# Kernel optimization log

Measured on AMD Instinct MI355X. Metric: run time of the kernel, lower is better.

The kernel has to match this reference:

```python
import jax, jax.numpy as jnp
import numpy as np

N_MODELS = 64
IN_F = 256
OUT_F = 256
BATCH = 8192


def setup_inputs() -> dict:
    key = jax.random.key(0)
    kx, kw, kb, ki = jax.random.split(key, 4)
    x = jax.random.normal(kx, (BATCH, OUT_F), dtype=jnp.float32)
    idxs = jax.random.randint(ki, (BATCH,), 0, N_MODELS, dtype=jnp.int64)
    # learned parameters (torch inits them to zeros; we use random so grads/outputs are nontrivial)
    w = jax.random.normal(kw, (N_MODELS, IN_F, OUT_F), dtype=jnp.float32) * 0.02
    b = jax.random.normal(kb, (N_MODELS, OUT_F), dtype=jnp.float32) * 0.02
    return {"x": x, "idxs": idxs, "w": w, "b": b}


def reference(x, idxs, w, b):
    # torch: baddbmm(b[idxs,:,None], w[idxs], x[:,:,None]).squeeze(-1) -> relu
    # y[n, i] = b[idxs[n], i] + sum_o w[idxs[n], i, o] * x[n, o]
    wg = w[idxs]                      # (B, in, out) gathered per-sample weights
    bg = b[idxs]                      # (B, out)
    y = jnp.einsum('bio,bo->bi', wg, x) + bg
    return jax.nn.relu(y)
```

## Files before the change

kernel.cpp:

```cpp
#include <hip/hip_runtime.h>
#include <stdint.h>


#define N_MODELS 64
#define IN_F     256
#define OUT_F    256
#define BATCH    8192
#define BM       128
#define BN       128
#define PKX      264

typedef __bf16 bf16x8 __attribute__((ext_vector_type(8)));
typedef float  f32x4  __attribute__((ext_vector_type(4)));
typedef __attribute__((address_space(3))) uint32_t lds_u32;
typedef const __attribute__((address_space(1))) uint32_t glb_u32;

__device__ __forceinline__ void dma16(const void* g, void* l) {
  __builtin_amdgcn_global_load_lds((glb_u32*)g, (lds_u32*)l, 16, 0, 0);
}

__device__ __forceinline__ bf16x8 pack8(float4 a, float4 b) {
  bf16x8 o;
  o[0] = (__bf16)a.x; o[1] = (__bf16)a.y; o[2] = (__bf16)a.z; o[3] = (__bf16)a.w;
  o[4] = (__bf16)b.x; o[5] = (__bf16)b.y; o[6] = (__bf16)b.z; o[7] = (__bf16)b.w;
  return o;
}

__global__ __launch_bounds__(1024) void compact_kernel(
    const int* __restrict__ idxs, int* __restrict__ rid_g,
    int* __restrict__ cnt_g) {
  const int model = blockIdx.x;
  const int t     = threadIdx.x;
  const int lane  = t & 63;
  const int wv    = t >> 6;
  __shared__ int wsum[16];

  const int4* ip = (const int4*)idxs + t * 2;
  int4 iv0 = ip[0], iv1 = ip[1];

  int cnt = (iv0.x == model) + (iv0.y == model) + (iv0.z == model) + (iv0.w == model)
          + (iv1.x == model) + (iv1.y == model) + (iv1.z == model) + (iv1.w == model);
  int inc = cnt;
#pragma unroll
  for (int d = 1; d < 64; d <<= 1) {
    int u = __shfl_up(inc, d);
    if (lane >= d) inc += u;
  }
  if (lane == 63) wsum[wv] = inc;
  __syncthreads();
  int wpre = 0, total = 0;
#pragma unroll
  for (int j = 0; j < 16; ++j) {
    int s = wsum[j];
    total += s;
    if (j < wv) wpre += s;
  }
  int off = wpre + inc - cnt;
  int* rg = rid_g + model * 256;
  {
    int n0 = t * 8;
    if (iv0.x == model) { if ((unsigned)off < 256u) rg[off] = n0 + 0; ++off; }
    if (iv0.y == model) { if ((unsigned)off < 256u) rg[off] = n0 + 1; ++off; }
    if (iv0.z == model) { if ((unsigned)off < 256u) rg[off] = n0 + 2; ++off; }
    if (iv0.w == model) { if ((unsigned)off < 256u) rg[off] = n0 + 3; ++off; }
    if (iv1.x == model) { if ((unsigned)off < 256u) rg[off] = n0 + 4; ++off; }
    if (iv1.y == model) { if ((unsigned)off < 256u) rg[off] = n0 + 5; ++off; }
    if (iv1.z == model) { if ((unsigned)off < 256u) rg[off] = n0 + 6; ++off; }
    if (iv1.w == model) { if ((unsigned)off < 256u) rg[off] = n0 + 7; ++off; }
  }
  if (t < 256 && t >= total) rg[t] = -1;
  if (t == 0) cnt_g[model] = total;
}

__global__ __launch_bounds__(1024) void gemm_kernel(
    const float* __restrict__ x, const float* __restrict__ w,
    const float* __restrict__ bias_g, float* __restrict__ out,
    const int* __restrict__ rid_g, const int* __restrict__ cnt_g) {
  const int b     = (blockIdx.x & 7) * 32 + (blockIdx.x >> 3);
  const int model = b >> 2;
  const int s     = (b >> 1) & 1;
  const int i0    = (b & 1) * BN;
  const int t     = threadIdx.x;
  const int lane  = t & 63;
  const int wv    = t >> 6;

  __shared__ float w_lds[2][BM][64];
  __shared__ unsigned short a_lds[BM][PKX];
  __shared__ int rid[BM];

  const int total = cnt_g[model];
  if (s * BM >= total) return;

  if (t < BM) rid[t] = rid_g[model * 256 + s * BM + t];
  const int rwx  = t >> 3;
  const int hx   = t & 7;
  const int srow = rid_g[model * 256 + s * BM + rwx];

  const float* wbase = w + (size_t)model * (IN_F * OUT_F) + (size_t)i0 * IN_F;
  const int l_r = lane >> 4;
  const int l_c = lane & 15;
#define W_DMA(q, buf)                                                        \
  {                                                                          \
    _Pragma("unroll")                                                        \
    for (int j = 0; j < 2; ++j) {                                            \
      const int r0 = wv * 8 + j * 4;                                         \
      const int rr = r0 + l_r;                                               \
      const float* gs = wbase + (size_t)rr * IN_F + (q) * 64                 \
                        + ((l_c ^ (rr & 7)) << 2);                           \
      dma16(gs, &w_lds[buf][r0][0]);                                         \
    }                                                                        \
  }

  W_DMA(0, 0)
  W_DMA(1, 1)

  const float* xrow = x + (size_t)(srow < 0 ? 0 : srow) * IN_F + hx * 32;
  {
    float4 tx[8];
#pragma unroll
    for (int j = 0; j < 8; ++j) tx[j] = *(const float4*)(xrow + j * 4);
#pragma unroll
    for (int j = 0; j < 4; ++j)
      *(bf16x8*)&a_lds[rwx][hx * 32 + j * 8] = pack8(tx[2 * j], tx[2 * j + 1]);
  }

  const int wm   = (wv & 3) * 32;
  const int wn   = (wv >> 2) * 32;
  const int col  = lane & 15;
  const int quad = lane >> 4;
  float bv[2];
  const float* bp = bias_g + model * OUT_F + i0 + wn + col;
#pragma unroll
  for (int nt = 0; nt < 2; ++nt) bv[nt] = bp[nt * 16];

  __syncthreads();

  f32x4 acc[2][2];
#pragma unroll
  for (int mt = 0; mt < 2; ++mt)
#pragma unroll
    for (int nt = 0; nt < 2; ++nt)
      acc[mt][nt] = (f32x4){bv[nt], bv[nt], bv[nt], bv[nt]};

#define MFMA_QUARTER(buf, ks0)                                               \
  {                                                                          \
    _Pragma("unroll")                                                        \
    for (int kk = 0; kk < 2; ++kk) {                                         \
      const int ks  = (ks0) + kk;                                            \
      const int ch0 = kk * 8 + quad * 2;                                     \
      bf16x8 af[2], bfr[2];                                                  \
      _Pragma("unroll")                                                      \
      for (int mt = 0; mt < 2; ++mt)                                         \
        af[mt] = *(const bf16x8*)&a_lds[wm + mt * 16 + col]                  \
                                      [ks * 32 + quad * 8];                  \
      _Pragma("unroll")                                                      \
      for (int nt = 0; nt < 2; ++nt) {                                       \
        const int R  = wn + nt * 16 + col;                                   \
        const int sw = R & 7;                                                \
        float4 f0 = *(const float4*)&w_lds[buf][R][((ch0)     ^ sw) << 2];   \
        float4 f1 = *(const float4*)&w_lds[buf][R][((ch0 + 1) ^ sw) << 2];   \
        bfr[nt] = pack8(f0, f1);                                             \
      }                                                                      \
      _Pragma("unroll")                                                      \
      for (int mt = 0; mt < 2; ++mt)                                         \
        _Pragma("unroll")                                                    \
        for (int nt = 0; nt < 2; ++nt)                                       \
          acc[mt][nt] = __builtin_amdgcn_mfma_f32_16x16x32_bf16(             \
              af[mt], bfr[nt], acc[mt][nt], 0, 0, 0);                        \
    }                                                                        \
  }

  MFMA_QUARTER(0, 0)
  __syncthreads();
  W_DMA(2, 0)
  MFMA_QUARTER(1, 2)
  __syncthreads();
  W_DMA(3, 1)
  MFMA_QUARTER(0, 4)
  __syncthreads();
  MFMA_QUARTER(1, 6)

#pragma unroll
  for (int mt = 0; mt < 2; ++mt) {
#pragma unroll
    for (int reg = 0; reg < 4; ++reg) {
      const int mm = wm + mt * 16 + quad * 4 + reg;
      const int sle = rid[mm];
      if (sle >= 0) {
        float* orow = out + (size_t)sle * OUT_F + i0 + wn + col;
#pragma unroll
        for (int nt = 0; nt < 2; ++nt)
          orow[nt * 16] = fmaxf(acc[mt][nt][reg], 0.0f);
      }
    }
  }
#undef W_DMA
#undef MFMA_QUARTER
}

extern "C" void kernel_launch(void* const* d_in, const int* in_sizes, int n_in,
                              void* d_out, int out_size, void* d_ws, size_t ws_size,
                              hipStream_t stream) {
  const float* x    = (const float*)d_in[0];
  const int*   idxs = (const int*)d_in[1];
  const float* w    = (const float*)d_in[2];
  const float* b    = (const float*)d_in[3];
  float* out = (float*)d_out;

  int* rid_g = (int*)d_ws;
  int* cnt_g = rid_g + N_MODELS * 256;

  compact_kernel<<<N_MODELS, 1024, 0, stream>>>(idxs, rid_g, cnt_g);
  gemm_kernel<<<N_MODELS * 4, 1024, 0, stream>>>(x, w, b, out, rid_g, cnt_g);
}
```

Baseline: 86.39 us.

## Fuse per-model index compaction into the grouped GEMM kernel

Removes the separate compaction kernel and its global workspace round trip. Each GEMM block now scans all indices itself, builds its row list in LDS, and then proceeds. The weight DMA prefetch is issued before the scan for the first sub-tile, and after the early-exit check for the second. This saves one launch and the dependency between the two kernels, but every block now redundantly scans all 8192 indices. Rows beyond 256 per model remain dropped, as before.

```diff
diff --git a/kernel.cpp b/kernel.cpp
--- a/kernel.cpp
+++ b/kernel.cpp
@@ -19,6 +19,12 @@
   __builtin_amdgcn_global_load_lds((glb_u32*)g, (lds_u32*)l, 16, 0, 0);
 }
 
+__device__ __forceinline__ void barrier_lds_only() {
+  asm volatile("s_waitcnt lgkmcnt(0)" ::: "memory");
+  __builtin_amdgcn_s_barrier();
+  __builtin_amdgcn_sched_barrier(0);
+}
+
 __device__ __forceinline__ bf16x8 pack8(float4 a, float4 b) {
   bf16x8 o;
   o[0] = (__bf16)a.x; o[1] = (__bf16)a.y; o[2] = (__bf16)a.z; o[3] = (__bf16)a.w;
@@ -26,56 +32,10 @@
   return o;
 }
 
-__global__ __launch_bounds__(1024) void compact_kernel(
-    const int* __restrict__ idxs, int* __restrict__ rid_g,
-    int* __restrict__ cnt_g) {
-  const int model = blockIdx.x;
-  const int t     = threadIdx.x;
-  const int lane  = t & 63;
-  const int wv    = t >> 6;
-  __shared__ int wsum[16];
-
-  const int4* ip = (const int4*)idxs + t * 2;
-  int4 iv0 = ip[0], iv1 = ip[1];
-
-  int cnt = (iv0.x == model) + (iv0.y == model) + (iv0.z == model) + (iv0.w == model)
-          + (iv1.x == model) + (iv1.y == model) + (iv1.z == model) + (iv1.w == model);
-  int inc = cnt;
-#pragma unroll
-  for (int d = 1; d < 64; d <<= 1) {
-    int u = __shfl_up(inc, d);
-    if (lane >= d) inc += u;
-  }
-  if (lane == 63) wsum[wv] = inc;
-  __syncthreads();
-  int wpre = 0, total = 0;
-#pragma unroll
-  for (int j = 0; j < 16; ++j) {
-    int s = wsum[j];
-    total += s;
-    if (j < wv) wpre += s;
-  }
-  int off = wpre + inc - cnt;
-  int* rg = rid_g + model * 256;
-  {
-    int n0 = t * 8;
-    if (iv0.x == model) { if ((unsigned)off < 256u) rg[off] = n0 + 0; ++off; }
-    if (iv0.y == model) { if ((unsigned)off < 256u) rg[off] = n0 + 1; ++off; }
-    if (iv0.z == model) { if ((unsigned)off < 256u) rg[off] = n0 + 2; ++off; }
-    if (iv0.w == model) { if ((unsigned)off < 256u) rg[off] = n0 + 3; ++off; }
-    if (iv1.x == model) { if ((unsigned)off < 256u) rg[off] = n0 + 4; ++off; }
-    if (iv1.y == model) { if ((unsigned)off < 256u) rg[off] = n0 + 5; ++off; }
-    if (iv1.z == model) { if ((unsigned)off < 256u) rg[off] = n0 + 6; ++off; }
-    if (iv1.w == model) { if ((unsigned)off < 256u) rg[off] = n0 + 7; ++off; }
-  }
-  if (t < 256 && t >= total) rg[t] = -1;
-  if (t == 0) cnt_g[model] = total;
-}
-
-__global__ __launch_bounds__(1024) void gemm_kernel(
-    const float* __restrict__ x, const float* __restrict__ w,
-    const float* __restrict__ bias_g, float* __restrict__ out,
-    const int* __restrict__ rid_g, const int* __restrict__ cnt_g) {
+__global__ __launch_bounds__(1024) void fused_kernel(
+    const float* __restrict__ x, const int* __restrict__ idxs,
+    const float* __restrict__ w, const float* __restrict__ bias_g,
+    float* __restrict__ out) {
   const int b     = (blockIdx.x & 7) * 32 + (blockIdx.x >> 3);
   const int model = b >> 2;
   const int s     = (b >> 1) & 1;
@@ -87,14 +47,10 @@
   __shared__ float w_lds[2][BM][64];
   __shared__ unsigned short a_lds[BM][PKX];
   __shared__ int rid[BM];
-
-  const int total = cnt_g[model];
-  if (s * BM >= total) return;
-
-  if (t < BM) rid[t] = rid_g[model * 256 + s * BM + t];
-  const int rwx  = t >> 3;
-  const int hx   = t & 7;
-  const int srow = rid_g[model * 256 + s * BM + rwx];
+  __shared__ int wsum[16];
+
+  const int4* ip = (const int4*)idxs + t * 2;
+  int4 iv0 = ip[0], iv1 = ip[1];
 
   const float* wbase = w + (size_t)model * (IN_F * OUT_F) + (size_t)i0 * IN_F;
   const int l_r = lane >> 4;
@@ -111,9 +67,48 @@
     }                                                                        \
   }
 
-  W_DMA(0, 0)
-  W_DMA(1, 1)
-
+  if (s == 0) { W_DMA(0, 0) W_DMA(1, 1) }
+
+  if (t < BM) rid[t] = -1;
+
+  int cnt = (iv0.x == model) + (iv0.y == model) + (iv0.z == model) + (iv0.w == model)
+          + (iv1.x == model) + (iv1.y == model) + (iv1.z == model) + (iv1.w == model);
+  int inc = cnt;
+#pragma unroll
+  for (int d = 1; d < 64; d <<= 1) {
+    int u = __shfl_up(inc, d);
+    if (lane >= d) inc += u;
+  }
+  if (lane == 63) wsum[wv] = inc;
+  barrier_lds_only();
+  int wpre = 0, total = 0;
+#pragma unroll
+  for (int j = 0; j < 16; ++j) {
+    int sj = wsum[j];
+    total += sj;
+    if (j < wv) wpre += sj;
+  }
+  const int start = s * BM;
+  if (start >= total) return;
+  if (s == 1) { W_DMA(0, 0) W_DMA(1, 1) }
+
+  int off = wpre + inc - cnt - start;
+  {
+    int n0 = t * 8;
+    if (iv0.x == model) { if ((unsigned)off < BM) rid[off] = n0 + 0; ++off; }
+    if (iv0.y == model) { if ((unsigned)off < BM) rid[off] = n0 + 1; ++off; }
+    if (iv0.z == model) { if ((unsigned)off < BM) rid[off] = n0 + 2; ++off; }
+    if (iv0.w == model) { if ((unsigned)off < BM) rid[off] = n0 + 3; ++off; }
+    if (iv1.x == model) { if ((unsigned)off < BM) rid[off] = n0 + 4; ++off; }
+    if (iv1.y == model) { if ((unsigned)off < BM) rid[off] = n0 + 5; ++off; }
+    if (iv1.z == model) { if ((unsigned)off < BM) rid[off] = n0 + 6; ++off; }
+    if (iv1.w == model) { if ((unsigned)off < BM) rid[off] = n0 + 7; ++off; }
+  }
+  barrier_lds_only();
+
+  const int rwx = t >> 3;
+  const int hx  = t & 7;
+  const int srow = rid[rwx];
   const float* xrow = x + (size_t)(srow < 0 ? 0 : srow) * IN_F + hx * 32;
   {
     float4 tx[8];
@@ -206,10 +201,7 @@
   const float* w    = (const float*)d_in[2];
   const float* b    = (const float*)d_in[3];
   float* out = (float*)d_out;
-
-  int* rid_g = (int*)d_ws;
-  int* cnt_g = rid_g + N_MODELS * 256;
-
-  compact_kernel<<<N_MODELS, 1024, 0, stream>>>(idxs, rid_g, cnt_g);
-  gemm_kernel<<<N_MODELS * 4, 1024, 0, stream>>>(x, w, b, out, rid_g, cnt_g);
-}
+  (void)d_ws; (void)ws_size;
+
+  fused_kernel<<<N_MODELS * 4, 1024, 0, stream>>>(x, idxs, w, b, out);
+}
```

Measured after the change: 86.20 us. No clear change (-0.2%).
